# Kernel tuning notes

Measured on AMD Instinct MI355X. Metric: run time of the kernel, lower is better.

The kernel has to match this reference:

```python
import jax, jax.numpy as jnp
import numpy as np

B, L, D = 4, 2048, 512
CHUNK = 64
EPS = 1e-5


def setup_inputs() -> dict:
    key = jax.random.key(0)
    kx, kw = jax.random.split(key)
    x = jax.random.normal(kx, (B, L, D), dtype=jnp.float32)
    W = jax.random.normal(kw, (D, D), dtype=jnp.float32) / np.float32(np.sqrt(D))
    return {
        "x": x,
        "W": W,
        "eta": jnp.asarray(0.01, jnp.float32),
        "lam_logit": jnp.asarray(np.log(0.99 / 0.01), jnp.float32),  # logit(0.99)
        "ln_gamma": jnp.ones((D,), jnp.float32),
        "ln_beta": jnp.zeros((D,), jnp.float32),
    }


def _gated_delta_scan(k, v, q, lam, beta):
    """Gated delta rule: S_t = lam*S_{t-1} + beta * k_t (x) (v_t - lam*S_{t-1}^T k_t);
    o_t = S_t^T q_t (scale=1.0, single head of dim D). k,v,q: [B,L,D] -> o: [B,L,D]."""
    b, l, d = k.shape
    nc = l // CHUNK

    def to_scan(t):  # [B,L,D] -> [nc, CHUNK, B, D]
        return t.transpose(1, 0, 2).reshape(nc, CHUNK, b, d)

    ks, vs, qs = to_scan(k), to_scan(v), to_scan(q)

    def step(S, inp):
        k_t, v_t, q_t = inp                      # each [B,D]
        S = lam * S                              # scalar decay exp(g), g = log(lam)
        v_err = beta * (v_t - jnp.einsum('bk,bkv->bv', k_t, S))
        S = S + k_t[:, :, None] * v_err[:, None, :]
        o_t = jnp.einsum('bk,bkv->bv', q_t, S)
        return S, o_t

    def chunk_body(S, ch):
        return jax.lax.scan(step, S, ch)

    S0 = jnp.zeros((b, d, d), k.dtype)
    _, o = jax.lax.scan(chunk_body, S0, (ks, vs, qs))  # o: [nc, CHUNK, B, D]
    return o.reshape(l, b, d).transpose(1, 0, 2)


def reference(x, W, eta, lam_logit, ln_gamma, ln_beta):
    lam = jax.nn.sigmoid(lam_logit)
    x_act = jnp.tanh(x)
    static_out = jnp.einsum('bld,ed->ble', x_act, W)  # torch Linear (no bias): x @ W.T
    # k = q = tanh(x), v = W @ tanh(x), g = log(lam), beta = eta
    o_dyn = _gated_delta_scan(x_act, static_out, x_act, lam, eta)
    y = static_out + o_dyn
    mu = jnp.mean(y, axis=-1, keepdims=True)
    var = jnp.var(y, axis=-1, keepdims=True)
    return (y - mu) * jax.lax.rsqrt(var + EPS) * ln_gamma + ln_beta
```

## Files before the change

### kernel.cpp

```cpp
#include <hip/hip_runtime.h>
#include <math.h>

#define BB 4
#define LL 2048
#define DD 512
#define CC 64
#define NC 32
#define VB 8
#define EPSF 1e-5f

typedef unsigned int u32;
typedef unsigned short u16;
typedef __attribute__((ext_vector_type(4))) u32 u32x4;
typedef __attribute__((ext_vector_type(4))) float f32x4;
typedef __attribute__((ext_vector_type(8))) __bf16 bf16x8;

__device__ __forceinline__ u16 f2bf(float f) {
  return __builtin_bit_cast(u16, (__bf16)f);
}
__device__ __forceinline__ int sx6(int s) { return (s ^ (s >> 3)) & 7; }
__device__ __forceinline__ bf16x8 ldf(const u16* p) {
  return __builtin_bit_cast(bf16x8, *(const u32x4*)p);
}
__device__ __forceinline__ bf16x8 bcv(u32x4 v) { return __builtin_bit_cast(bf16x8, v); }

__device__ __forceinline__ void gld16(u16* lds, const u16* g) {
  __builtin_amdgcn_global_load_lds(
      (const __attribute__((address_space(1))) u32*)g,
      (__attribute__((address_space(3))) u32*)lds, 16, 0, 0);
}
__device__ __forceinline__ void barrier_lgkm() {
  asm volatile("s_waitcnt lgkmcnt(0)" ::: "memory");
  __builtin_amdgcn_sched_barrier(0);
  __builtin_amdgcn_s_barrier();
  __builtin_amdgcn_sched_barrier(0);
}
__device__ __forceinline__ void barrier_all() {
  asm volatile("s_waitcnt vmcnt(0) lgkmcnt(0)" ::: "memory");
  __builtin_amdgcn_sched_barrier(0);
  __builtin_amdgcn_s_barrier();
  __builtin_amdgcn_sched_barrier(0);
}

__global__ __launch_bounds__(256) void k_cvtW(const float* __restrict__ W,
                                              u16* __restrict__ wbb) {
  int idx = (blockIdx.x * 256 + threadIdx.x) * 8;
  float4 a = *(const float4*)(W + idx);
  float4 b = *(const float4*)(W + idx + 4);
  float v[8] = {a.x, a.y, a.z, a.w, b.x, b.y, b.z, b.w};
  u32x4 pk;
#pragma unroll
  for (int j = 0; j < 4; ++j)
    pk[j] = (u32)f2bf(v[2 * j]) | ((u32)f2bf(v[2 * j + 1]) << 16);
  *(u32x4*)(wbb + idx) = pk;
}

__global__ __launch_bounds__(256) void k_prep3(const float* __restrict__ x,
                                               const float* __restrict__ eta_p,
                                               const float* __restrict__ ll_p,
                                               u16* __restrict__ kbs,
                                               u16* __restrict__ tbs,
                                               u16* __restrict__ tcs,
                                               u16* __restrict__ p1g,
                                               u16* __restrict__ p2g,
                                               u16* __restrict__ kbt) {
  __shared__ __align__(16) u16 Kl[CC * DD];
  __shared__ float Gl[64 * 64];
  __shared__ float Gs[64 * 64];
  __shared__ float Tl[64 * 65];
  __shared__ __align__(16) u16 MtL[64 * 64];
  __shared__ __align__(16) u16 TbT[64 * 64];
  __shared__ __align__(16) u16 TcT[64 * 64];
  __shared__ float pw[72];
  int bc = blockIdx.x;
  int b = bc >> 5, c = bc & 31;
  int tid = threadIdx.x;
  int wid = tid >> 6, lane = tid & 63;
  int lo = lane & 15, hi = lane >> 4;
  float beta = *eta_p;
  float lam = 1.f / (1.f + expf(-*ll_p));
  if (tid <= 64) pw[tid] = powf(lam, (float)tid);
  for (int i = tid; i < 64 * 65; i += 256) Tl[i] = 0.f;
  const float* xg = x + (size_t)(b * LL + c * CC) * DD;
  u16* kbs_c = kbs + (size_t)(b * LL + c * CC) * DD;
#pragma unroll
  for (int i = 0; i < 16; ++i) {
    int idx = tid + i * 256;
    int r = idx >> 6, k8 = (idx & 63) * 8;
    const float* xp = xg + (size_t)r * DD + k8;
    float4 a = *(const float4*)xp;
    float4 b4 = *(const float4*)(xp + 4);
    float v[8] = {a.x, a.y, a.z, a.w, b4.x, b4.y, b4.z, b4.w};
    u32x4 pk;
#pragma unroll
    for (int j = 0; j < 4; ++j)
      pk[j] = (u32)f2bf(tanhf(v[2 * j])) | ((u32)f2bf(tanhf(v[2 * j + 1])) << 16);
    int off = r * DD + (k8 ^ (sx6(r) << 3));
    *(u32x4*)(Kl + off) = pk;
    *(u32x4*)(kbs_c + off) = pk;
  }
  __syncthreads();
  {
    f32x4 acc[4] = {{0.f,0.f,0.f,0.f},{0.f,0.f,0.f,0.f},{0.f,0.f,0.f,0.f},{0.f,0.f,0.f,0.f}};
    int t = 16 * wid + lo;
    int mT = sx6(t) << 3;
#pragma unroll
    for (int kq = 0; kq < 16; ++kq) {
      int col = hi * 8 + kq * 32;
      bf16x8 aF = ldf(Kl + t * DD + (col ^ mT));
#pragma unroll
      for (int sb = 0; sb < 4; ++sb) {
        int s = 16 * sb + lo;
        bf16x8 bF = ldf(Kl + s * DD + (col ^ (sx6(s) << 3)));
        acc[sb] = __builtin_amdgcn_mfma_f32_16x16x32_bf16(aF, bF, acc[sb], 0, 0, 0);
      }
    }
#pragma unroll
    for (int sb = 0; sb < 4; ++sb)
#pragma unroll
      for (int r = 0; r < 4; ++r)
        Gl[(16 * wid + 4 * hi + r) * 64 + 16 * sb + lo] = acc[sb][r];
  }
  __syncthreads();
#pragma unroll
  for (int i = 0; i < 16; ++i) {
    int idx = tid + i * 256;
    int tq = idx >> 6, sq = idx & 63;
    Gs[idx] = (sq < tq) ? beta * pw[tq - sq] * Gl[idx] : 0.f;
  }
  __syncthreads();
  {
    int q = hi;
    int j = 16 * wid + lo;
    for (int t = 0; t < 64; ++t) {
      float ps = 0.f;
#pragma unroll
      for (int i = 0; i < 16; ++i) {
        int s = 16 * q + i;
        ps = fmaf(Gs[t * 64 + s], Tl[s * 65 + j], ps);
      }
      ps += __shfl_xor(ps, 16, 64);
      ps += __shfl_xor(ps, 32, 64);
      if (q == 0) Tl[t * 65 + j] = ((t == j) ? 1.f : 0.f) - ps;
    }
  }
  __syncthreads();
  u16* tbso = tbs + (size_t)bc * 4096;
  u16* tcso = tcs + (size_t)bc * 4096;
#pragma unroll
  for (int i = 0; i < 16; ++i) {
    int idx = tid + i * 256;
    int s = idx >> 6, r = idx & 63;
    float tv = Tl[s * 65 + r];
    float sc = pw[63 - s] * beta;
    tbso[idx] = f2bf(sc * tv);
    tcso[idx] = f2bf(-sc * pw[r + 1] * tv);
    int swz = r ^ (sx6(s) << 3);
    float mtv = (r < s) ? pw[s - r] * Gl[s * 64 + r]
                        : ((r == s) ? Gl[s * 64 + r] : 0.f);
    MtL[s * 64 + swz] = f2bf(mtv);
    float tvT = Tl[r * 65 + s];
    TbT[s * 64 + swz] = f2bf(beta * tvT);
    TcT[s * 64 + swz] = f2bf(-beta * pw[s + 1] * tvT);
  }
  __syncthreads();
  {
    f32x4 p1a[4], p2a[4];
#pragma unroll
    for (int rt = 0; rt < 4; ++rt) {
      p1a[rt] = (f32x4){0.f, 0.f, 0.f, 0.f};
      p2a[rt] = (f32x4){0.f, 0.f, 0.f, 0.f};
    }
    int srow = 16 * wid + lo;
    int aswz = sx6(srow) << 3;
#pragma unroll
    for (int km = 0; km < 2; ++km) {
      int mo = hi * 8 + km * 32;
      bf16x8 aF = ldf(MtL + srow * 64 + (mo ^ aswz));
#pragma unroll
      for (int rt = 0; rt < 4; ++rt) {
        int rrow = 16 * rt + lo;
        int bswz = sx6(rrow) << 3;
        p1a[rt] = __builtin_amdgcn_mfma_f32_16x16x32_bf16(
            aF, ldf(TbT + rrow * 64 + (mo ^ bswz)), p1a[rt], 0, 0, 0);
        p2a[rt] = __builtin_amdgcn_mfma_f32_16x16x32_bf16(
            aF, ldf(TcT + rrow * 64 + (mo ^ bswz)), p2a[rt], 0, 0, 0);
      }
    }
    u16* p1o = p1g + (size_t)bc * 4096;
    u16* p2o = p2g + (size_t)bc * 4096;
#pragma unroll
    for (int rt = 0; rt < 4; ++rt)
#pragma unroll
      for (int rg = 0; rg < 4; ++rg) {
        int s = 16 * wid + 4 * hi + rg;
        int r = 16 * rt + lo;
        p1o[s * 64 + r] = f2bf(p1a[rt][rg]);
        p2o[s * 64 + r] = f2bf(p2a[rt][rg]);
      }
  }
  u16* ktb = kbt + (size_t)bc * CC * DD;
#pragma unroll
  for (int rr = 0; rr < 2; ++rr) {
    int k = rr * 256 + tid;
    int kbase = k & ~7, klo = k & 7;
    int mk = sx6(k) << 3;
#pragma unroll
    for (int g = 0; g < 8; ++g) {
      u32 w4[4];
#pragma unroll
      for (int p = 0; p < 4; ++p) {
        int s0 = g * 8 + 2 * p;
        u16 e0 = Kl[s0 * DD + (kbase ^ (sx6(s0) << 3)) + klo];
        u16 e1 = Kl[(s0 + 1) * DD + (kbase ^ (sx6(s0 + 1) << 3)) + klo];
        w4[p] = (u32)e0 | ((u32)e1 << 16);
      }
      *(u32x4*)(ktb + (size_t)k * 64 + ((8 * g) ^ mk)) = (u32x4){w4[0], w4[1], w4[2], w4[3]};
    }
  }
}

__global__ __launch_bounds__(512, 2) void k_scan9(const u16* __restrict__ kbs,
                                                  const u16* __restrict__ kbt,
                                                  const u16* __restrict__ wbb,
                                                  const u16* __restrict__ tbs,
                                                  const u16* __restrict__ tcs,
                                                  const u16* __restrict__ p1g,
                                                  const u16* __restrict__ p2g,
                                                  const float* __restrict__ ll_p,
                                                  float* __restrict__ y) {
  __shared__ __align__(16) u16 Sb[16 * DD];
  __shared__ __align__(16) float Up[2][64][20];
  __shared__ __align__(16) u16 Vt[16 * 64];
  __shared__ __align__(16) u16 Ut[16 * 64];
  __shared__ __align__(16) u16 Ws[16 * 64];

  int b = blockIdx.x >> 6;
  int vb = blockIdx.x & 63;
  int v0 = vb * VB;
  int tid = threadIdx.x;
  int wid = tid >> 6, lane = tid & 63;
  int wq = wid & 3, kh = wid >> 2;
  int lo = lane & 15, hi = lane >> 4;
  int sidx = 16 * wq + lo;
  int mS = sx6(sidx) << 3;
  int mLo = sx6(lo) << 3;
  int kOff = kh * 256;

  float lam = 1.f / (1.f + expf(-*ll_p));
  float lam64 = powf(lam, 64.f);
  float csc = powf(lam, (float)(sidx + 1));

  {
    u32x4 z = {0u, 0u, 0u, 0u};
    *((u32x4*)Sb + tid) = z;
    if (tid < 384) {
      u16* base = (tid >> 7) == 0 ? Vt : (tid >> 7) == 1 ? Ut : Ws;
      *((u32x4*)base + (tid & 127)) = z;
    }
    int r8 = wid;
    u32x4 wrow = *(const u32x4*)(wbb + (size_t)(v0 + r8) * DD + lane * 8);
    *(u32x4*)(Sb + (size_t)(8 + r8) * DD + ((lane * 8) ^ (sx6(8 + r8) << 3))) = wrow;
  }
  const u16* kb_b = kbs + (size_t)b * LL * DD;
  float* yb = y + (size_t)b * LL * DD;

  u32x4 kB[8];
#pragma unroll
  for (int kq = 0; kq < 8; ++kq)
    kB[kq] = *(const u32x4*)(kb_b + (size_t)sidx * DD +
                             ((kOff + hi * 8 + kq * 32) ^ mS));
  u32x4 kt0[4], kt1[4], fA0, fA1, fB0, fB1;
  {
    const u16* ktc = kbt + (size_t)(b * NC + 0) * CC * DD;
#pragma unroll
    for (int t = 0; t < 4; ++t) {
      int k = 16 * (4 * wid + t) + lo;
      const u16* rowp = ktc + (size_t)k * 64;
      int m = sx6(k) << 3;
      kt0[t] = *(const u32x4*)(rowp + ((8 * hi) ^ m));
      kt1[t] = *(const u32x4*)(rowp + ((8 * hi + 32) ^ m));
    }
    size_t tbase = ((size_t)(b * NC + 0) * 64 + sidx) * 64 + hi * 8;
    const u16* mA = (kh == 0) ? tbs : p1g;
    const u16* mB = (kh == 0) ? tcs : p2g;
    fA0 = *(const u32x4*)(mA + tbase);
    fA1 = *(const u32x4*)(mA + tbase + 32);
    fB0 = *(const u32x4*)(mB + tbase);
    fB1 = *(const u32x4*)(mB + tbase + 32);
  }
  f32x4 Sa[4];
#pragma unroll
  for (int t = 0; t < 4; ++t) Sa[t] = (f32x4){0.f, 0.f, 0.f, 0.f};
  barrier_all();

  for (int c = 0; c < NC; ++c) {
    {
      f32x4 A0 = {0.f,0.f,0.f,0.f}, A1 = {0.f,0.f,0.f,0.f};
#pragma unroll
      for (int kq = 0; kq < 8; ++kq) {
        int col = kOff + hi * 8 + kq * 32;
        bf16x8 sA = ldf(Sb + lo * DD + (col ^ mLo));
        if (kq & 1) A1 = __builtin_amdgcn_mfma_f32_16x16x32_bf16(sA, bcv(kB[kq]), A1, 0, 0, 0);
        else        A0 = __builtin_amdgcn_mfma_f32_16x16x32_bf16(sA, bcv(kB[kq]), A0, 0, 0, 0);
      }
      f32x4 F = A0 + A1;
      *(f32x4*)&Up[kh][sidx][4 * hi] = F;
    }
    barrier_lgkm();
    if (c + 1 < NC) {
      const u16* src = kb_b + ((size_t)(c + 1) * CC + sidx) * DD;
#pragma unroll
      for (int kq = 0; kq < 8; ++kq)
        kB[kq] = *(const u32x4*)(src + ((kOff + hi * 8 + kq * 32) ^ mS));
    }
    f32x4 Fr;
    {
      f32x4 a = *(const f32x4*)&Up[0][sidx][4 * hi];
      f32x4 bq = *(const f32x4*)&Up[1][sidx][4 * hi];
      Fr = a + bq;
      if (kh == 0) {
        if (hi < 2) {
#pragma unroll
          for (int r = 0; r < 4; ++r) {
            int m = 4 * hi + r;
            Ut[m * 64 + (sidx ^ (sx6(m) << 3))] = f2bf(Fr[r]);
          }
        } else {
#pragma unroll
          for (int r = 0; r < 4; ++r) {
            int m = 4 * hi + r - 8;
            Vt[m * 64 + (sidx ^ (sx6(m) << 3))] = f2bf(Fr[r]);
          }
        }
      }
    }
    barrier_lgkm();
    {
      bf16x8 vf0 = ldf(Vt + lo * 64 + ((hi * 8) ^ mLo));
      bf16x8 vf1 = ldf(Vt + lo * 64 + ((hi * 8 + 32) ^ mLo));
      bf16x8 uf0 = ldf(Ut + lo * 64 + ((hi * 8) ^ mLo));
      bf16x8 uf1 = ldf(Ut + lo * 64 + ((hi * 8 + 32) ^ mLo));
      if (kh == 0) {
        f32x4 Wa0 = {0.f,0.f,0.f,0.f}, Wa1 = {0.f,0.f,0.f,0.f};
        Wa0 = __builtin_amdgcn_mfma_f32_16x16x32_bf16(vf0, bcv(fA0), Wa0, 0, 0, 0);
        Wa1 = __builtin_amdgcn_mfma_f32_16x16x32_bf16(vf1, bcv(fA1), Wa1, 0, 0, 0);
        Wa0 = __builtin_amdgcn_mfma_f32_16x16x32_bf16(uf0, bcv(fB0), Wa0, 0, 0, 0);
        Wa1 = __builtin_amdgcn_mfma_f32_16x16x32_bf16(uf1, bcv(fB1), Wa1, 0, 0, 0);
        f32x4 Wa = Wa0 + Wa1;
        if (hi < 2) {
#pragma unroll
          for (int r = 0; r < 4; ++r) {
            int v = 4 * hi + r;
            Ws[v * 64 + (sidx ^ (sx6(v) << 3))] = f2bf(Wa[r]);
          }
        }
      } else {
        f32x4 Vsw;
#pragma unroll
        for (int r = 0; r < 4; ++r) Vsw[r] = __shfl_xor(Fr[r], 32, 64);
        f32x4 Oa, Ob = {0.f,0.f,0.f,0.f};
#pragma unroll
        for (int r = 0; r < 4; ++r) Oa[r] = (hi < 2) ? csc * Fr[r] : 0.f;
        Oa = __builtin_amdgcn_mfma_f32_16x16x32_bf16(vf0, bcv(fA0), Oa, 0, 0, 0);
        Ob = __builtin_amdgcn_mfma_f32_16x16x32_bf16(vf1, bcv(fA1), Ob, 0, 0, 0);
        Oa = __builtin_amdgcn_mfma_f32_16x16x32_bf16(uf0, bcv(fB0), Oa, 0, 0, 0);
        Ob = __builtin_amdgcn_mfma_f32_16x16x32_bf16(uf1, bcv(fB1), Ob, 0, 0, 0);
        if (hi < 2) {
          float4 yo = make_float4(Vsw[0] + Oa[0] + Ob[0], Vsw[1] + Oa[1] + Ob[1],
                                  Vsw[2] + Oa[2] + Ob[2], Vsw[3] + Oa[3] + Ob[3]);
          *(float4*)(yb + (size_t)(c * CC + sidx) * DD + v0 + 4 * hi) = yo;
        }
      }
    }
    barrier_lgkm();
    {
      bf16x8 ws0 = ldf(Ws + lo * 64 + ((hi * 8) ^ mLo));
      bf16x8 ws1 = ldf(Ws + lo * 64 + ((hi * 8 + 32) ^ mLo));
#pragma unroll
      for (int t = 0; t < 4; ++t) {
        f32x4 acc = Sa[t] * lam64;
        acc = __builtin_amdgcn_mfma_f32_16x16x32_bf16(ws0, bcv(kt0[t]), acc, 0, 0, 0);
        acc = __builtin_amdgcn_mfma_f32_16x16x32_bf16(ws1, bcv(kt1[t]), acc, 0, 0, 0);
        Sa[t] = acc;
      }
      if (hi < 2) {
#pragma unroll
        for (int t = 0; t < 4; ++t) {
          int kc = 16 * (4 * wid + t) + lo;
#pragma unroll
          for (int r = 0; r < 4; ++r) {
            int v = 4 * hi + r;
            Sb[v * DD + (kc ^ (sx6(v) << 3))] = f2bf(Sa[t][r]);
          }
        }
      }
    }
    if (c + 1 < NC) {
      const u16* ktc = kbt + (size_t)(b * NC + c + 1) * CC * DD;
#pragma unroll
      for (int t = 0; t < 4; ++t) {
        int k = 16 * (4 * wid + t) + lo;
        const u16* rowp = ktc + (size_t)k * 64;
        int m = sx6(k) << 3;
        kt0[t] = *(const u32x4*)(rowp + ((8 * hi) ^ m));
        kt1[t] = *(const u32x4*)(rowp + ((8 * hi + 32) ^ m));
      }
      size_t tbase = ((size_t)(b * NC + c + 1) * 64 + sidx) * 64 + hi * 8;
      const u16* mA = (kh == 0) ? tbs : p1g;
      const u16* mB = (kh == 0) ? tcs : p2g;
      fA0 = *(const u32x4*)(mA + tbase);
      fA1 = *(const u32x4*)(mA + tbase + 32);
      fB0 = *(const u32x4*)(mB + tbase);
      fB1 = *(const u32x4*)(mB + tbase + 32);
    }
    barrier_lgkm();
  }
}

__global__ __launch_bounds__(256) void k_ln(float* __restrict__ y,
                                            const float* __restrict__ gamma,
                                            const float* __restrict__ lbeta) {
  int row = blockIdx.x * 4 + (threadIdx.x >> 6);
  int lane = threadIdx.x & 63;
  float* yr = y + (size_t)row * DD + lane * 8;
  float4 a = *(const float4*)yr;
  float4 b = *(const float4*)(yr + 4);
  float v[8] = {a.x, a.y, a.z, a.w, b.x, b.y, b.z, b.w};
  float s = 0.f, ss = 0.f;
#pragma unroll
  for (int j = 0; j < 8; ++j) {
    s += v[j];
    ss = fmaf(v[j], v[j], ss);
  }
#pragma unroll
  for (int m = 1; m < 64; m <<= 1) {
    s += __shfl_xor(s, m, 64);
    ss += __shfl_xor(ss, m, 64);
  }
  float mu = s * (1.f / DD);
  float var = ss * (1.f / DD) - mu * mu;
  float inv = rsqrtf(var + EPSF);
  const float* gp = gamma + lane * 8;
  const float* bp = lbeta + lane * 8;
  float4 g0 = *(const float4*)gp;
  float4 g1 = *(const float4*)(gp + 4);
  float4 b0 = *(const float4*)bp;
  float4 b1 = *(const float4*)(bp + 4);
  float g[8] = {g0.x, g0.y, g0.z, g0.w, g1.x, g1.y, g1.z, g1.w};
  float bb[8] = {b0.x, b0.y, b0.z, b0.w, b1.x, b1.y, b1.z, b1.w};
#pragma unroll
  for (int j = 0; j < 8; ++j) v[j] = (v[j] - mu) * inv * g[j] + bb[j];
  *(float4*)yr = make_float4(v[0], v[1], v[2], v[3]);
  *(float4*)(yr + 4) = make_float4(v[4], v[5], v[6], v[7]);
}

extern "C" void kernel_launch(void* const* d_in, const int* in_sizes, int n_in,
                              void* d_out, int out_size, void* d_ws, size_t ws_size,
                              hipStream_t stream) {
  const float* x     = (const float*)d_in[0];
  const float* W     = (const float*)d_in[1];
  const float* eta   = (const float*)d_in[2];
  const float* ll    = (const float*)d_in[3];
  const float* gamma = (const float*)d_in[4];
  const float* lbeta = (const float*)d_in[5];
  float* out = (float*)d_out;

  u16* kbs = (u16*)d_ws;
  u16* kbt = kbs + (size_t)BB * LL * DD;
  u16* wbb = kbt + (size_t)BB * LL * DD;
  u16* tbs = wbb + (size_t)DD * DD;
  u16* tcs = tbs + (size_t)BB * NC * 64 * 64;
  u16* p1g = tcs + (size_t)BB * NC * 64 * 64;
  u16* p2g = p1g + (size_t)BB * NC * 64 * 64;

  k_cvtW<<<128, 256, 0, stream>>>(W, wbb);
  k_prep3<<<BB * NC, 256, 0, stream>>>(x, eta, ll, kbs, tbs, tcs, p1g, p2g, kbt);
  k_scan9<<<256, 512, 0, stream>>>(kbs, kbt, wbb, tbs, tcs, p1g, p2g, ll, out);
  k_ln<<<2048, 256, 0, stream>>>(out, gamma, lbeta);
}
```

Measured before the change: 149.7 us.

## Fold identity and decay terms into prep matrices, drop cross-half reduction barrier

The prep kernel adds an identity diagonal to one projection matrix and a lambda-power diagonal to the other. This lets the scan kernel skip the explicit direct-value and decay-scaled terms. Each k-half now writes its own partial U/V tiles in bf16 to separate LDS buffers, and the MFMAs sum over both halves. That removes the fp32 Up reduction buffer and one barrier per chunk. Both wave groups then compute the same product, with one group writing Ws and the other writing the output. In exchange, partial sums are rounded to bf16 before they are combined, and the MFMA work in that stage doubles.

```diff
diff --git a/kernel.cpp b/kernel.cpp
--- a/kernel.cpp
+++ b/kernel.cpp
@@ -195,8 +195,10 @@
       for (int rg = 0; rg < 4; ++rg) {
         int s = 16 * wid + 4 * hi + rg;
         int r = 16 * rt + lo;
-        p1o[s * 64 + r] = f2bf(p1a[rt][rg]);
-        p2o[s * 64 + r] = f2bf(p2a[rt][rg]);
+        float d1 = (s == r) ? 1.f : 0.f;
+        float d2 = (s == r) ? pw[s + 1] : 0.f;
+        p1o[s * 64 + r] = f2bf(p1a[rt][rg] + d1);
+        p2o[s * 64 + r] = f2bf(p2a[rt][rg] + d2);
       }
   }
   u16* ktb = kbt + (size_t)bc * CC * DD;
@@ -220,7 +222,7 @@
   }
 }
 
-__global__ __launch_bounds__(512, 2) void k_scan9(const u16* __restrict__ kbs,
+__global__ __launch_bounds__(512, 2) void k_scanC(const u16* __restrict__ kbs,
                                                   const u16* __restrict__ kbt,
                                                   const u16* __restrict__ wbb,
                                                   const u16* __restrict__ tbs,
@@ -230,9 +232,8 @@
                                                   const float* __restrict__ ll_p,
                                                   float* __restrict__ y) {
   __shared__ __align__(16) u16 Sb[16 * DD];
-  __shared__ __align__(16) float Up[2][64][20];
-  __shared__ __align__(16) u16 Vt[16 * 64];
-  __shared__ __align__(16) u16 Ut[16 * 64];
+  __shared__ __align__(16) u16 Ut2[2][16 * 64];
+  __shared__ __align__(16) u16 Vt2[2][16 * 64];
   __shared__ __align__(16) u16 Ws[16 * 64];
 
   int b = blockIdx.x >> 6;
@@ -249,18 +250,20 @@
 
   float lam = 1.f / (1.f + expf(-*ll_p));
   float lam64 = powf(lam, 64.f);
-  float csc = powf(lam, (float)(sidx + 1));
 
   {
     u32x4 z = {0u, 0u, 0u, 0u};
-    *((u32x4*)Sb + tid) = z;
-    if (tid < 384) {
-      u16* base = (tid >> 7) == 0 ? Vt : (tid >> 7) == 1 ? Ut : Ws;
-      *((u32x4*)base + (tid & 127)) = z;
-    }
-    int r8 = wid;
-    u32x4 wrow = *(const u32x4*)(wbb + (size_t)(v0 + r8) * DD + lane * 8);
-    *(u32x4*)(Sb + (size_t)(8 + r8) * DD + ((lane * 8) ^ (sx6(8 + r8) << 3))) = wrow;
+    ((u32x4*)Sb)[tid] = z;
+    if (tid < 256) {
+      ((u32x4*)Ut2)[tid] = z;
+      ((u32x4*)Vt2)[tid] = z;
+    }
+    if (tid < 128) ((u32x4*)Ws)[tid] = z;
+    if (wid < 8 && wid >= 0) {}
+    if (wid < 8) {
+      u32x4 wrow = *(const u32x4*)(wbb + (size_t)(v0 + wid) * DD + lane * 8);
+      *(u32x4*)(Sb + (size_t)(8 + wid) * DD + ((lane * 8) ^ (sx6(8 + wid) << 3))) = wrow;
+    }
   }
   const u16* kb_b = kbs + (size_t)b * LL * DD;
   float* yb = y + (size_t)b * LL * DD;
@@ -305,49 +308,42 @@
         else        A0 = __builtin_amdgcn_mfma_f32_16x16x32_bf16(sA, bcv(kB[kq]), A0, 0, 0, 0);
       }
       f32x4 F = A0 + A1;
-      *(f32x4*)&Up[kh][sidx][4 * hi] = F;
-    }
-    barrier_lgkm();
+      if (hi < 2) {
+#pragma unroll
+        for (int r = 0; r < 4; ++r) {
+          int m = 4 * hi + r;
+          Ut2[kh][m * 64 + (sidx ^ (sx6(m) << 3))] = f2bf(F[r]);
+        }
+      } else {
+#pragma unroll
+        for (int r = 0; r < 4; ++r) {
+          int m = 4 * hi + r - 8;
+          Vt2[kh][m * 64 + (sidx ^ (sx6(m) << 3))] = f2bf(F[r]);
+        }
+      }
+    }
     if (c + 1 < NC) {
       const u16* src = kb_b + ((size_t)(c + 1) * CC + sidx) * DD;
 #pragma unroll
       for (int kq = 0; kq < 8; ++kq)
         kB[kq] = *(const u32x4*)(src + ((kOff + hi * 8 + kq * 32) ^ mS));
     }
-    f32x4 Fr;
-    {
-      f32x4 a = *(const f32x4*)&Up[0][sidx][4 * hi];
-      f32x4 bq = *(const f32x4*)&Up[1][sidx][4 * hi];
-      Fr = a + bq;
-      if (kh == 0) {
-        if (hi < 2) {
-#pragma unroll
-          for (int r = 0; r < 4; ++r) {
-            int m = 4 * hi + r;
-            Ut[m * 64 + (sidx ^ (sx6(m) << 3))] = f2bf(Fr[r]);
-          }
-        } else {
-#pragma unroll
-          for (int r = 0; r < 4; ++r) {
-            int m = 4 * hi + r - 8;
-            Vt[m * 64 + (sidx ^ (sx6(m) << 3))] = f2bf(Fr[r]);
-          }
-        }
-      }
-    }
     barrier_lgkm();
     {
-      bf16x8 vf0 = ldf(Vt + lo * 64 + ((hi * 8) ^ mLo));
-      bf16x8 vf1 = ldf(Vt + lo * 64 + ((hi * 8 + 32) ^ mLo));
-      bf16x8 uf0 = ldf(Ut + lo * 64 + ((hi * 8) ^ mLo));
-      bf16x8 uf1 = ldf(Ut + lo * 64 + ((hi * 8 + 32) ^ mLo));
-      if (kh == 0) {
-        f32x4 Wa0 = {0.f,0.f,0.f,0.f}, Wa1 = {0.f,0.f,0.f,0.f};
+      f32x4 Wa0 = {0.f,0.f,0.f,0.f}, Wa1 = {0.f,0.f,0.f,0.f};
+#pragma unroll
+      for (int h = 0; h < 2; ++h) {
+        bf16x8 vf0 = ldf(Vt2[h] + lo * 64 + ((hi * 8) ^ mLo));
+        bf16x8 vf1 = ldf(Vt2[h] + lo * 64 + ((hi * 8 + 32) ^ mLo));
+        bf16x8 uf0 = ldf(Ut2[h] + lo * 64 + ((hi * 8) ^ mLo));
+        bf16x8 uf1 = ldf(Ut2[h] + lo * 64 + ((hi * 8 + 32) ^ mLo));
         Wa0 = __builtin_amdgcn_mfma_f32_16x16x32_bf16(vf0, bcv(fA0), Wa0, 0, 0, 0);
         Wa1 = __builtin_amdgcn_mfma_f32_16x16x32_bf16(vf1, bcv(fA1), Wa1, 0, 0, 0);
         Wa0 = __builtin_amdgcn_mfma_f32_16x16x32_bf16(uf0, bcv(fB0), Wa0, 0, 0, 0);
         Wa1 = __builtin_amdgcn_mfma_f32_16x16x32_bf16(uf1, bcv(fB1), Wa1, 0, 0, 0);
-        f32x4 Wa = Wa0 + Wa1;
+      }
+      f32x4 Wa = Wa0 + Wa1;
+      if (kh == 0) {
         if (hi < 2) {
 #pragma unroll
           for (int r = 0; r < 4; ++r) {
@@ -356,19 +352,8 @@
           }
         }
       } else {
-        f32x4 Vsw;
-#pragma unroll
-        for (int r = 0; r < 4; ++r) Vsw[r] = __shfl_xor(Fr[r], 32, 64);
-        f32x4 Oa, Ob = {0.f,0.f,0.f,0.f};
-#pragma unroll
-        for (int r = 0; r < 4; ++r) Oa[r] = (hi < 2) ? csc * Fr[r] : 0.f;
-        Oa = __builtin_amdgcn_mfma_f32_16x16x32_bf16(vf0, bcv(fA0), Oa, 0, 0, 0);
-        Ob = __builtin_amdgcn_mfma_f32_16x16x32_bf16(vf1, bcv(fA1), Ob, 0, 0, 0);
-        Oa = __builtin_amdgcn_mfma_f32_16x16x32_bf16(uf0, bcv(fB0), Oa, 0, 0, 0);
-        Ob = __builtin_amdgcn_mfma_f32_16x16x32_bf16(uf1, bcv(fB1), Ob, 0, 0, 0);
         if (hi < 2) {
-          float4 yo = make_float4(Vsw[0] + Oa[0] + Ob[0], Vsw[1] + Oa[1] + Ob[1],
-                                  Vsw[2] + Oa[2] + Ob[2], Vsw[3] + Oa[3] + Ob[3]);
+          float4 yo = make_float4(Wa[0], Wa[1], Wa[2], Wa[3]);
           *(float4*)(yb + (size_t)(c * CC + sidx) * DD + v0 + 4 * hi) = yo;
         }
       }
@@ -476,6 +461,6 @@
 
   k_cvtW<<<128, 256, 0, stream>>>(W, wbb);
   k_prep3<<<BB * NC, 256, 0, stream>>>(x, eta, ll, kbs, tbs, tcs, p1g, p2g, kbt);
-  k_scan9<<<256, 512, 0, stream>>>(kbs, kbt, wbb, tbs, tcs, p1g, p2g, ll, out);
+  k_scanC<<<256, 512, 0, stream>>>(kbs, kbt, wbb, tbs, tcs, p1g, p2g, ll, out);
   k_ln<<<2048, 256, 0, stream>>>(out, gamma, lbeta);
 }
```

Result: faster. 146.4 us (-2.2%).
